# Kernel optimization log

Measured on AMD Instinct MI355X. Metric: run time of the kernel, lower is better.

## Reference

```python
import jax, jax.numpy as jnp
import numpy as np


def setup_inputs() -> dict:
    key = jax.random.key(0)
    k1, k2 = jax.random.split(key)
    B, N, M, D = 8, 8192, 8192, 3
    x = jax.random.normal(k1, (B, N, D), dtype=jnp.float32)
    y = jax.random.normal(k2, (B, M, D), dtype=jnp.float32)
    return {"x": x, "y": y}


def reference(x, y):
    # dist[b, i, j] = |x_bi|^2 + |y_bj|^2 - 2 * <x_bi, y_bj>
    # (same math as the torch code's rx.transpose(2,1) + ry - 2*xy, but
    #  computed with row-norm vectors instead of full NxN / MxM bmms)
    xx = jnp.sum(x * x, axis=-1)                      # [B, N]
    yy = jnp.sum(y * y, axis=-1)                      # [B, M]
    xy = jnp.einsum('bnd,bmd->bnm', x, y)             # [B, N, M]
    dist = xx[:, :, None] + yy[:, None, :] - 2.0 * xy # [B, N, M]
    dist1 = jnp.min(dist, axis=1)  # min over x points -> per-y nearest  [B, M]
    dist2 = jnp.min(dist, axis=2)  # min over y points -> per-x nearest  [B, N]
    return jnp.mean(dist1) + jnp.mean(dist2)
```

## Files before the change

### kernel.cpp

```cpp
#include <hip/hip_runtime.h>


#define B_ 8
#define N_ 8192
#define PTS (B_ * N_)
#define ROWS_TOTAL (2 * PTS)
#define NTILES 2048
#define TPB 256

typedef short bf16x8 __attribute__((ext_vector_type(8)));
typedef float f32x16 __attribute__((ext_vector_type(16)));

__device__ __forceinline__ unsigned b16(float f) {
  unsigned u = __float_as_uint(f);
  return (u + 0x7FFFu + ((u >> 16) & 1u)) >> 16;
}
__device__ __forceinline__ float bf(unsigned h) { return __uint_as_float(h << 16); }

__global__ __launch_bounds__(256) void pack_frags_k(
    const float* __restrict__ x, const float* __restrict__ y,
    uint4* __restrict__ afrag, uint4* __restrict__ bfrag) {
  const unsigned one = 0x3F80u;
  int t = blockIdx.x * 256 + threadIdx.x;
  int kind = t >> 17;
  int dir = (t >> 16) & 1;
  int p = t & 65535;
  int tile = dir * NTILES + (p >> 5), m = p & 31;
  if (kind == 0) {
    const float* src = dir ? y : x;
    const float* po = src + 3 * p;
    float v0 = po[0], v1 = po[1], v2 = po[2];
    float nv = fmaf(v0, v0, fmaf(v1, v1, v2 * v2));
    float a0 = -2.0f * v0, a1 = -2.0f * v1, a2 = -2.0f * v2;
    unsigned ah0 = b16(a0), ah1 = b16(a1), ah2 = b16(a2);
    unsigned al0 = b16(a0 - bf(ah0)), al1 = b16(a1 - bf(ah1)), al2 = b16(a2 - bf(ah2));
    unsigned nh = b16(nv), nl = b16(nv - bf(nh));
    afrag[tile * 64 + m]      = make_uint4(ah0 | (ah1 << 16), ah2 | (ah0 << 16),
                                           ah1 | (ah2 << 16), al0 | (al1 << 16));
    afrag[tile * 64 + 32 + m] = make_uint4(al2 | (nh << 16), nl | (one << 16), one, 0u);
  } else {
    const float* src = dir ? x : y;
    const float* pc = src + 3 * p;
    float c0 = pc[0], c1 = pc[1], c2 = pc[2];
    float nc = fmaf(c0, c0, fmaf(c1, c1, c2 * c2));
    unsigned yh0 = b16(c0), yh1 = b16(c1), yh2 = b16(c2);
    unsigned yl0 = b16(c0 - bf(yh0)), yl1 = b16(c1 - bf(yh1)), yl2 = b16(c2 - bf(yh2));
    unsigned nh = b16(nc), nl = b16(nc - bf(nh));
    bfrag[tile * 64 + m]      = make_uint4(yh0 | (yh1 << 16), yh2 | (yl0 << 16),
                                           yl1 | (yl2 << 16), yh0 | (yh1 << 16));
    bfrag[tile * 64 + 32 + m] = make_uint4(yh2 | (one << 16), one | (nh << 16), nl, 0u);
  }
}

__global__ __launch_bounds__(TPB, 3) void chamfer_main_k(
    const uint4* __restrict__ afrag, const uint4* __restrict__ bfrag,
    float* __restrict__ gpart) {
  int t = threadIdx.x, lane = t & 63, w = t >> 6;
  int b0 = blockIdx.x;
  int eff = ((b0 & 7) << 8) | (b0 >> 3);
  int q = eff & 3;
  int rg = eff >> 2;
  int dir = rg >> 8;
  int batch = (rg >> 5) & 7;
  int rb = rg & 31;

  int tileA0 = dir * NTILES + batch * 256 + rb * 8 + w * 2;
  bf16x8 A0 = __builtin_bit_cast(bf16x8, afrag[tileA0 * 64 + lane]);
  bf16x8 A1 = __builtin_bit_cast(bf16x8, afrag[(tileA0 + 1) * 64 + lane]);

  const uint4* bt = bfrag + (size_t)(dir * NTILES + batch * 256 + q * 64) * 64 + lane;

  f32x16 z, rm0, rm1;
#pragma unroll
  for (int r = 0; r < 16; ++r) { z[r] = 0.0f; rm0[r] = 1e30f; rm1[r] = 1e30f; }

#pragma unroll 2
  for (int j = 0; j < 64; j += 2) {
    bf16x8 B0 = __builtin_bit_cast(bf16x8, bt[(j    ) * 64]);
    bf16x8 B1 = __builtin_bit_cast(bf16x8, bt[(j + 1) * 64]);
    f32x16 acc0 = __builtin_amdgcn_mfma_f32_32x32x16_bf16(A0, B0, z, 0, 0, 0);
    f32x16 acc1 = __builtin_amdgcn_mfma_f32_32x32x16_bf16(A1, B0, z, 0, 0, 0);
    f32x16 acc2 = __builtin_amdgcn_mfma_f32_32x32x16_bf16(A0, B1, z, 0, 0, 0);
    f32x16 acc3 = __builtin_amdgcn_mfma_f32_32x32x16_bf16(A1, B1, z, 0, 0, 0);
#pragma unroll
    for (int r = 0; r < 16; ++r) {
      rm0[r] = fminf(fminf(rm0[r], acc0[r]), acc2[r]);
      rm1[r] = fminf(fminf(rm1[r], acc1[r]), acc3[r]);
    }
  }

#pragma unroll
  for (int msk = 1; msk <= 16; msk <<= 1)
#pragma unroll
    for (int r = 0; r < 16; ++r) {
      rm0[r] = fminf(rm0[r], __shfl_xor(rm0[r], msk, 64));
      rm1[r] = fminf(rm1[r], __shfl_xor(rm1[r], msk, 64));
    }

  int rowbase = dir * PTS + batch * N_ + rb * 256 + w * 64;
  float* gp = gpart + q * ROWS_TOTAL + rowbase;
  if ((lane & 31) == 0) {
    int h = lane >> 5;
#pragma unroll
    for (int r = 0; r < 16; ++r) {
      int rr = (r & 3) + 8 * (r >> 2) + 4 * h;
      gp[rr] = rm0[r];
      gp[32 + rr] = rm1[r];
    }
  }
}

__global__ __launch_bounds__(256) void chamfer_final_k(
    const float* __restrict__ gpart, float* __restrict__ out) {
  int i = blockIdx.x * 256 + threadIdx.x;
  const float4* g4 = reinterpret_cast<const float4*>(gpart);
  float4 a = g4[i];
  float4 b = g4[i + (ROWS_TOTAL / 4)];
  float4 c = g4[i + 2 * (ROWS_TOTAL / 4)];
  float4 d = g4[i + 3 * (ROWS_TOTAL / 4)];
  float s = fminf(fminf(a.x, b.x), fminf(c.x, d.x))
          + fminf(fminf(a.y, b.y), fminf(c.y, d.y))
          + fminf(fminf(a.z, b.z), fminf(c.z, d.z))
          + fminf(fminf(a.w, b.w), fminf(c.w, d.w));
  for (int off = 32; off > 0; off >>= 1) s += __shfl_down(s, off, 64);
  __shared__ float red[4];
  int lane = threadIdx.x & 63, wv = threadIdx.x >> 6;
  if (lane == 0) red[wv] = s;
  __syncthreads();
  if (threadIdx.x == 0) {
    float tt = (red[0] + red[1]) + (red[2] + red[3]);
    atomicAdd(out, tt * (1.0f / (float)PTS));
  }
}

extern "C" void kernel_launch(void* const* d_in, const int* in_sizes, int n_in,
                              void* d_out, int out_size, void* d_ws, size_t ws_size,
                              hipStream_t stream) {
  const float* x = (const float*)d_in[0];
  const float* y = (const float*)d_in[1];
  float* out = (float*)d_out;
  float* gpart = (float*)d_ws;
  uint4* afrag = (uint4*)((char*)d_ws + (size_t)4 * ROWS_TOTAL * sizeof(float));
  uint4* bfrag = afrag + (size_t)2 * NTILES * 64;

  hipMemsetAsync(out, 0, sizeof(float), stream);
  pack_frags_k<<<1024, 256, 0, stream>>>(x, y, afrag, bfrag);
  chamfer_main_k<<<2048, TPB, 0, stream>>>(afrag, bfrag, gpart);
  chamfer_final_k<<<128, 256, 0, stream>>>(gpart, out);
}
```

Measured before the change: 103.3 us.

## Fuse final reduction into main kernel via last-block arrival counter

Removes the separate final reduction kernel and the memset. Output zeroing and flag reset move into the pack kernel. In the main kernel, each row group counts its four column-quarter blocks with an atomic counter, and the last block to arrive merges the partial minima and atomically adds the sum. This saves two launches and their gaps, at the cost of fences, an atomic per block, and a tail merge on the critical path.

```diff
diff --git a/kernel.cpp b/kernel.cpp
--- a/kernel.cpp
+++ b/kernel.cpp
@@ -6,6 +6,7 @@
 #define PTS (B_ * N_)
 #define ROWS_TOTAL (2 * PTS)
 #define NTILES 2048
+#define NRG 512
 #define TPB 256
 
 typedef short bf16x8 __attribute__((ext_vector_type(8)));
@@ -17,11 +18,18 @@
 }
 __device__ __forceinline__ float bf(unsigned h) { return __uint_as_float(h << 16); }
 
+__device__ __forceinline__ float devload(const float* p) {
+  return __hip_atomic_load(p, __ATOMIC_RELAXED, __HIP_MEMORY_SCOPE_AGENT);
+}
+
 __global__ __launch_bounds__(256) void pack_frags_k(
     const float* __restrict__ x, const float* __restrict__ y,
-    uint4* __restrict__ afrag, uint4* __restrict__ bfrag) {
+    uint4* __restrict__ afrag, uint4* __restrict__ bfrag,
+    int* __restrict__ flags, float* __restrict__ out) {
   const unsigned one = 0x3F80u;
   int t = blockIdx.x * 256 + threadIdx.x;
+  if (t < NRG) flags[t] = 0;
+  if (t == 0) *out = 0.0f;
   int kind = t >> 17;
   int dir = (t >> 16) & 1;
   int p = t & 65535;
@@ -54,7 +62,11 @@
 
 __global__ __launch_bounds__(TPB, 3) void chamfer_main_k(
     const uint4* __restrict__ afrag, const uint4* __restrict__ bfrag,
-    float* __restrict__ gpart) {
+    float* __restrict__ gpart, int* __restrict__ flags,
+    float* __restrict__ out) {
+  __shared__ int doMerge;
+  __shared__ float red[4];
+
   int t = threadIdx.x, lane = t & 63, w = t >> 6;
   int b0 = blockIdx.x;
   int eff = ((b0 & 7) << 8) | (b0 >> 3);
@@ -74,20 +86,22 @@
 #pragma unroll
   for (int r = 0; r < 16; ++r) { z[r] = 0.0f; rm0[r] = 1e30f; rm1[r] = 1e30f; }
 
+#define LD(ti) __builtin_bit_cast(bf16x8, bt[(ti) * 64])
+#define MF(Aa, Bb) __builtin_amdgcn_mfma_f32_32x32x16_bf16(Aa, Bb, z, 0, 0, 0)
+
 #pragma unroll 2
   for (int j = 0; j < 64; j += 2) {
-    bf16x8 B0 = __builtin_bit_cast(bf16x8, bt[(j    ) * 64]);
-    bf16x8 B1 = __builtin_bit_cast(bf16x8, bt[(j + 1) * 64]);
-    f32x16 acc0 = __builtin_amdgcn_mfma_f32_32x32x16_bf16(A0, B0, z, 0, 0, 0);
-    f32x16 acc1 = __builtin_amdgcn_mfma_f32_32x32x16_bf16(A1, B0, z, 0, 0, 0);
-    f32x16 acc2 = __builtin_amdgcn_mfma_f32_32x32x16_bf16(A0, B1, z, 0, 0, 0);
-    f32x16 acc3 = __builtin_amdgcn_mfma_f32_32x32x16_bf16(A1, B1, z, 0, 0, 0);
+    bf16x8 B0 = LD(j), B1 = LD(j + 1);
+    f32x16 a0 = MF(A0, B0), a1 = MF(A1, B0);
+    f32x16 a2 = MF(A0, B1), a3 = MF(A1, B1);
 #pragma unroll
     for (int r = 0; r < 16; ++r) {
-      rm0[r] = fminf(fminf(rm0[r], acc0[r]), acc2[r]);
-      rm1[r] = fminf(fminf(rm1[r], acc1[r]), acc3[r]);
+      rm0[r] = fminf(fminf(rm0[r], a0[r]), a2[r]);
+      rm1[r] = fminf(fminf(rm1[r], a1[r]), a3[r]);
     }
   }
+#undef LD
+#undef MF
 
 #pragma unroll
   for (int msk = 1; msk <= 16; msk <<= 1)
@@ -97,8 +111,8 @@
       rm1[r] = fminf(rm1[r], __shfl_xor(rm1[r], msk, 64));
     }
 
-  int rowbase = dir * PTS + batch * N_ + rb * 256 + w * 64;
-  float* gp = gpart + q * ROWS_TOTAL + rowbase;
+  int rgbase = dir * PTS + batch * N_ + rb * 256;
+  float* gp = gpart + (size_t)q * ROWS_TOTAL + rgbase + w * 64;
   if ((lane & 31) == 0) {
     int h = lane >> 5;
 #pragma unroll
@@ -108,28 +122,26 @@
       gp[32 + rr] = rm1[r];
     }
   }
-}
 
-__global__ __launch_bounds__(256) void chamfer_final_k(
-    const float* __restrict__ gpart, float* __restrict__ out) {
-  int i = blockIdx.x * 256 + threadIdx.x;
-  const float4* g4 = reinterpret_cast<const float4*>(gpart);
-  float4 a = g4[i];
-  float4 b = g4[i + (ROWS_TOTAL / 4)];
-  float4 c = g4[i + 2 * (ROWS_TOTAL / 4)];
-  float4 d = g4[i + 3 * (ROWS_TOTAL / 4)];
-  float s = fminf(fminf(a.x, b.x), fminf(c.x, d.x))
-          + fminf(fminf(a.y, b.y), fminf(c.y, d.y))
-          + fminf(fminf(a.z, b.z), fminf(c.z, d.z))
-          + fminf(fminf(a.w, b.w), fminf(c.w, d.w));
-  for (int off = 32; off > 0; off >>= 1) s += __shfl_down(s, off, 64);
-  __shared__ float red[4];
-  int lane = threadIdx.x & 63, wv = threadIdx.x >> 6;
-  if (lane == 0) red[wv] = s;
+  __threadfence();
+  if (t == 0)
+    doMerge = (atomicAdd(&flags[rg], 1) == 3) ? 1 : 0;
   __syncthreads();
-  if (threadIdx.x == 0) {
-    float tt = (red[0] + red[1]) + (red[2] + red[3]);
-    atomicAdd(out, tt * (1.0f / (float)PTS));
+  if (doMerge) {
+    __threadfence();
+    int row = rgbase + t;
+    float v0 = devload(gpart + 0 * (size_t)ROWS_TOTAL + row);
+    float v1 = devload(gpart + 1 * (size_t)ROWS_TOTAL + row);
+    float v2 = devload(gpart + 2 * (size_t)ROWS_TOTAL + row);
+    float v3 = devload(gpart + 3 * (size_t)ROWS_TOTAL + row);
+    float s = fminf(fminf(v0, v1), fminf(v2, v3));
+    for (int off = 32; off > 0; off >>= 1) s += __shfl_down(s, off, 64);
+    if (lane == 0) red[w] = s;
+    __syncthreads();
+    if (t == 0) {
+      float tt = (red[0] + red[1]) + (red[2] + red[3]);
+      atomicAdd(out, tt * (1.0f / (float)PTS));
+    }
   }
 }
 
@@ -139,12 +151,11 @@
   const float* x = (const float*)d_in[0];
   const float* y = (const float*)d_in[1];
   float* out = (float*)d_out;
-  float* gpart = (float*)d_ws;
-  uint4* afrag = (uint4*)((char*)d_ws + (size_t)4 * ROWS_TOTAL * sizeof(float));
+  int* flags = (int*)d_ws;
+  float* gpart = (float*)((char*)d_ws + 4096);
+  uint4* afrag = (uint4*)((char*)gpart + (size_t)4 * ROWS_TOTAL * sizeof(float));
   uint4* bfrag = afrag + (size_t)2 * NTILES * 64;
 
-  hipMemsetAsync(out, 0, sizeof(float), stream);
-  pack_frags_k<<<1024, 256, 0, stream>>>(x, y, afrag, bfrag);
-  chamfer_main_k<<<2048, TPB, 0, stream>>>(afrag, bfrag, gpart);
-  chamfer_final_k<<<128, 256, 0, stream>>>(gpart, out);
+  pack_frags_k<<<1024, 256, 0, stream>>>(x, y, afrag, bfrag, flags, out);
+  chamfer_main_k<<<2048, TPB, 0, stream>>>(afrag, bfrag, gpart, flags, out);
 }
```

Measured after the change: 258.9 us. 151% more time.

## Give each wave four A tiles to reuse B loads; fold memset into pack

Applied to the files above, without the earlier changes.

Each wave now holds four A fragment tiles instead of two, so every pair of B tiles loaded from global memory feeds eight MFMAs rather than four. The grid is halved to 1024 blocks to match, and the block index decode and output row mapping are updated. The separate memset of the output is replaced by thread 0 of the pack kernel zeroing it, which removes one stream operation. The extra running-min registers raise register pressure and may lower occupancy, and the smaller grid gives fewer blocks per CU.

```diff
diff --git a/kernel.cpp b/kernel.cpp
--- a/kernel.cpp
+++ b/kernel.cpp
@@ -19,9 +19,11 @@
 
 __global__ __launch_bounds__(256) void pack_frags_k(
     const float* __restrict__ x, const float* __restrict__ y,
-    uint4* __restrict__ afrag, uint4* __restrict__ bfrag) {
+    uint4* __restrict__ afrag, uint4* __restrict__ bfrag,
+    float* __restrict__ out) {
   const unsigned one = 0x3F80u;
   int t = blockIdx.x * 256 + threadIdx.x;
+  if (t == 0) *out = 0.0f;
   int kind = t >> 17;
   int dir = (t >> 16) & 1;
   int p = t & 65535;
@@ -57,37 +59,48 @@
     float* __restrict__ gpart) {
   int t = threadIdx.x, lane = t & 63, w = t >> 6;
   int b0 = blockIdx.x;
-  int eff = ((b0 & 7) << 8) | (b0 >> 3);
+  int eff = ((b0 & 7) << 7) | (b0 >> 3);
   int q = eff & 3;
   int rg = eff >> 2;
-  int dir = rg >> 8;
-  int batch = (rg >> 5) & 7;
-  int rb = rg & 31;
+  int dir = rg >> 7;
+  int batch = (rg >> 4) & 7;
+  int rb = rg & 15;
 
-  int tileA0 = dir * NTILES + batch * 256 + rb * 8 + w * 2;
-  bf16x8 A0 = __builtin_bit_cast(bf16x8, afrag[tileA0 * 64 + lane]);
+  int tileA0 = dir * NTILES + batch * 256 + rb * 16 + w * 4;
+  bf16x8 A0 = __builtin_bit_cast(bf16x8, afrag[(tileA0 + 0) * 64 + lane]);
   bf16x8 A1 = __builtin_bit_cast(bf16x8, afrag[(tileA0 + 1) * 64 + lane]);
+  bf16x8 A2 = __builtin_bit_cast(bf16x8, afrag[(tileA0 + 2) * 64 + lane]);
+  bf16x8 A3 = __builtin_bit_cast(bf16x8, afrag[(tileA0 + 3) * 64 + lane]);
 
   const uint4* bt = bfrag + (size_t)(dir * NTILES + batch * 256 + q * 64) * 64 + lane;
 
-  f32x16 z, rm0, rm1;
+  f32x16 z, rm0, rm1, rm2, rm3;
 #pragma unroll
-  for (int r = 0; r < 16; ++r) { z[r] = 0.0f; rm0[r] = 1e30f; rm1[r] = 1e30f; }
+  for (int r = 0; r < 16; ++r) {
+    z[r] = 0.0f;
+    rm0[r] = 1e30f; rm1[r] = 1e30f; rm2[r] = 1e30f; rm3[r] = 1e30f;
+  }
+
+#define LD(ti) __builtin_bit_cast(bf16x8, bt[(ti) * 64])
+#define MF(Aa, Bb) __builtin_amdgcn_mfma_f32_32x32x16_bf16(Aa, Bb, z, 0, 0, 0)
 
 #pragma unroll 2
   for (int j = 0; j < 64; j += 2) {
-    bf16x8 B0 = __builtin_bit_cast(bf16x8, bt[(j    ) * 64]);
-    bf16x8 B1 = __builtin_bit_cast(bf16x8, bt[(j + 1) * 64]);
-    f32x16 acc0 = __builtin_amdgcn_mfma_f32_32x32x16_bf16(A0, B0, z, 0, 0, 0);
-    f32x16 acc1 = __builtin_amdgcn_mfma_f32_32x32x16_bf16(A1, B0, z, 0, 0, 0);
-    f32x16 acc2 = __builtin_amdgcn_mfma_f32_32x32x16_bf16(A0, B1, z, 0, 0, 0);
-    f32x16 acc3 = __builtin_amdgcn_mfma_f32_32x32x16_bf16(A1, B1, z, 0, 0, 0);
+    bf16x8 B0 = LD(j), B1 = LD(j + 1);
+    f32x16 a00 = MF(A0, B0), a01 = MF(A0, B1);
+    f32x16 a10 = MF(A1, B0), a11 = MF(A1, B1);
+    f32x16 a20 = MF(A2, B0), a21 = MF(A2, B1);
+    f32x16 a30 = MF(A3, B0), a31 = MF(A3, B1);
 #pragma unroll
     for (int r = 0; r < 16; ++r) {
-      rm0[r] = fminf(fminf(rm0[r], acc0[r]), acc2[r]);
-      rm1[r] = fminf(fminf(rm1[r], acc1[r]), acc3[r]);
+      rm0[r] = fminf(fminf(rm0[r], a00[r]), a01[r]);
+      rm1[r] = fminf(fminf(rm1[r], a10[r]), a11[r]);
+      rm2[r] = fminf(fminf(rm2[r], a20[r]), a21[r]);
+      rm3[r] = fminf(fminf(rm3[r], a30[r]), a31[r]);
     }
   }
+#undef LD
+#undef MF
 
 #pragma unroll
   for (int msk = 1; msk <= 16; msk <<= 1)
@@ -95,17 +108,21 @@
     for (int r = 0; r < 16; ++r) {
       rm0[r] = fminf(rm0[r], __shfl_xor(rm0[r], msk, 64));
       rm1[r] = fminf(rm1[r], __shfl_xor(rm1[r], msk, 64));
+      rm2[r] = fminf(rm2[r], __shfl_xor(rm2[r], msk, 64));
+      rm3[r] = fminf(rm3[r], __shfl_xor(rm3[r], msk, 64));
     }
 
-  int rowbase = dir * PTS + batch * N_ + rb * 256 + w * 64;
-  float* gp = gpart + q * ROWS_TOTAL + rowbase;
+  int rowbase = dir * PTS + batch * N_ + rb * 512 + w * 128;
+  float* gp = gpart + (size_t)q * ROWS_TOTAL + rowbase;
   if ((lane & 31) == 0) {
     int h = lane >> 5;
 #pragma unroll
     for (int r = 0; r < 16; ++r) {
       int rr = (r & 3) + 8 * (r >> 2) + 4 * h;
-      gp[rr] = rm0[r];
-      gp[32 + rr] = rm1[r];
+      gp[0 * 32 + rr] = rm0[r];
+      gp[1 * 32 + rr] = rm1[r];
+      gp[2 * 32 + rr] = rm2[r];
+      gp[3 * 32 + rr] = rm3[r];
     }
   }
 }
@@ -143,8 +160,7 @@
   uint4* afrag = (uint4*)((char*)d_ws + (size_t)4 * ROWS_TOTAL * sizeof(float));
   uint4* bfrag = afrag + (size_t)2 * NTILES * 64;
 
-  hipMemsetAsync(out, 0, sizeof(float), stream);
-  pack_frags_k<<<1024, 256, 0, stream>>>(x, y, afrag, bfrag);
-  chamfer_main_k<<<2048, TPB, 0, stream>>>(afrag, bfrag, gpart);
+  pack_frags_k<<<1024, 256, 0, stream>>>(x, y, afrag, bfrag, out);
+  chamfer_main_k<<<1024, TPB, 0, stream>>>(afrag, bfrag, gpart);
   chamfer_final_k<<<128, 256, 0, stream>>>(gpart, out);
 }
```

Measured after the change: 239.9 us. +132.1%, slower.
